# Performance work log

Hardware: AMD Instinct MI355X
Metric: run time of the kernel (lower is better)

Reference implementation:

```python
import jax, jax.numpy as jnp
import numpy as np

STRIDE = 4
HEADS = 8
KSIZE = 5
PAD_L = 4  # causal: kernel_size - 1


def _layernorm(x, g, b, eps=1e-5):
    mu = jnp.mean(x, axis=-1, keepdims=True)
    var = jnp.mean((x - mu) ** 2, axis=-1, keepdims=True)
    return (x - mu) * jax.lax.rsqrt(var + eps) * g + b


def setup_inputs() -> dict:
    key = jax.random.key(0)
    ks = jax.random.split(key, 6)
    B, T, C = 8, 2048, 1024
    D = 4096
    x = jax.random.normal(ks[0], (B, T, C), dtype=jnp.float32)
    W_proj = jax.random.normal(ks[1], (C * STRIDE, D), dtype=jnp.float32) * 0.02
    b_proj = jnp.zeros((D,), dtype=jnp.float32)
    ln_g = jnp.ones((D,), dtype=jnp.float32)
    ln_b = jnp.zeros((D,), dtype=jnp.float32)
    W_wgen = jax.random.normal(ks[2], (D, HEADS * KSIZE), dtype=jnp.float32) * 0.02
    b_wgen = jnp.zeros((HEADS * KSIZE,), dtype=jnp.float32)
    W_ff = jax.random.normal(ks[3], (D, D), dtype=jnp.float32) * 0.02
    b_ff = jnp.zeros((D,), dtype=jnp.float32)
    return {"x": x, "W_proj": W_proj, "b_proj": b_proj, "ln_g": ln_g, "ln_b": ln_b,
            "W_wgen": W_wgen, "b_wgen": b_wgen, "W_ff": W_ff, "b_ff": b_ff}


def reference(x, W_proj, b_proj, ln_g, ln_b, W_wgen, b_wgen, W_ff, b_ff):
    B, T, C = x.shape
    folded_T = T // STRIDE
    # fold time into channels, then dense projection to llm_dim
    xf = x[:, : folded_T * STRIDE].reshape(B, folded_T, C * STRIDE)
    h = xf @ W_proj + b_proj  # [B, Tf, D]
    D = h.shape[-1]
    R = D // HEADS
    # LConv1DBlock with norm_before + dynamic conv + (linear, relu, dropout p=0) + residual
    res = h
    y = _layernorm(h, ln_g, ln_b)
    # per-position dynamic weights, softmax over kernel taps
    w = (y @ W_wgen + b_wgen).reshape(B, folded_T, HEADS, KSIZE)
    w = jax.nn.softmax(w, axis=-1)  # [B, Tf, H, K]
    # causal depthwise conv: out[t] = sum_k w[t,k] * y[t - (K-1) + k]
    yp = jnp.pad(y, ((0, 0), (PAD_L, 0), (0, 0)))  # left pad time
    # stacked taps: [K, B, Tf, H, R]
    taps = jnp.stack([yp[:, k:k + folded_T] for k in range(KSIZE)], axis=0)
    taps = taps.reshape(KSIZE, B, folded_T, HEADS, R)
    conv = jnp.einsum('kbthr,bthk->bthr', taps, w).reshape(B, folded_T, D)
    # feed-forward ops: linear -> relu -> dropout(p=0)
    out = res + jax.nn.relu(conv @ W_ff + b_ff)
    return out
```

## Files before the change

### kernel.cpp

```cpp
#include <hip/hip_runtime.h>

typedef unsigned short u16;
typedef unsigned int u32;
typedef __attribute__((ext_vector_type(8))) short bf16x8;
typedef __attribute__((ext_vector_type(4))) float f32x4;

__device__ __forceinline__ float bf2f(u16 u) {
    union { u32 i; float f; } x; x.i = ((u32)u) << 16; return x.f;
}
__device__ __forceinline__ u16 f2bf(float f) {
    union { float f; u32 i; } x; x.f = f;
    u32 u = x.i;
    u += 0x7FFFu + ((u >> 16) & 1u);
    return (u16)(u >> 16);
}
__device__ __forceinline__ float wred(float v) {
    #pragma unroll
    for (int off = 32; off; off >>= 1) v += __shfl_down(v, off);
    return v;
}
__device__ __forceinline__ void gload_lds16(const void* g, void* l) {
    __builtin_amdgcn_global_load_lds(
        (const __attribute__((address_space(1))) u32*)g,
        (__attribute__((address_space(3))) u32*)l,
        16, 0, 0);
}

__global__ __launch_bounds__(256)
void prep(const float* __restrict__ x, u16* __restrict__ xb,
          const float* __restrict__ Wp, u16* __restrict__ WpT,
          const float* __restrict__ Wf, u16* __restrict__ WfT,
          const float* __restrict__ Wg, float* __restrict__ WgT) {
    __shared__ float tile[64][65];
    int b = blockIdx.x;
    int tid = threadIdx.x;
    if (b < 16384) {
        int i = (b * 256 + tid) * 4;
        float4 v = *(const float4*)(x + i);
        ushort4 p;
        p.x = f2bf(v.x); p.y = f2bf(v.y); p.z = f2bf(v.z); p.w = f2bf(v.w);
        *(ushort4*)(xb + i) = p;
    } else if (b < 24576) {
        const float* W = (b < 20480) ? Wp : Wf;
        u16* Wt = (b < 20480) ? WpT : WfT;
        int bid = (b < 20480) ? (b - 16384) : (b - 20480);
        int n0 = (bid & 63) * 64;
        int k0 = (bid >> 6) * 64;
        int tx = tid & 31, ty = tid >> 5;
        #pragma unroll
        for (int i = 0; i < 8; ++i) {
            int kk = ty + i * 8;
            const float* src = W + (size_t)(k0 + kk) * 4096 + n0;
            tile[kk][tx]      = src[tx];
            tile[kk][tx + 32] = src[tx + 32];
        }
        __syncthreads();
        #pragma unroll
        for (int i = 0; i < 8; ++i) {
            int nn = ty + i * 8;
            ushort2 p;
            p.x = f2bf(tile[tx * 2][nn]);
            p.y = f2bf(tile[tx * 2 + 1][nn]);
            *(ushort2*)(Wt + (size_t)(n0 + nn) * 4096 + k0 + tx * 2) = p;
        }
    } else {
        int idx = (b - 24576) * 256 + tid;
        int c = idx >> 12, e = idx & 4095;
        WgT[idx] = Wg[(size_t)e * 40 + c];
    }
}

template <int MODE>
__global__ __launch_bounds__(512, 2)
void gemm256(const u16* __restrict__ A, const u16* __restrict__ Bt,
             const float* __restrict__ bias, const void* __restrict__ res,
             void* __restrict__ outv) {
    const int K = 4096, N = 4096;
    __shared__ u16 smem[65536];

    const int tid = threadIdx.x;
    const int lane = tid & 63;
    const int w = tid >> 6;
    const int wr = w >> 2, wc = w & 3;
    const int fr = lane & 15;
    const int fk = (lane >> 4) * 8;
    const int cswz = (fr & 7) << 3;

    const int bid = blockIdx.x;
    const int swz = (bid & 7) * (gridDim.x >> 3) + (bid >> 3);
    const int tm = swz >> 4, tn = swz & 15;
    const size_t rowA0 = (size_t)tm * 256;
    const size_t rowB0 = (size_t)tn * 256;

    const int srl = lane >> 3;
    const int scl = ((lane & 7) ^ srl) << 3;

    f32x4 acc[8][4] = {};
    bf16x8 af[8];
    bf16x8 bh0[4];
    bf16x8 bh1[4];

    auto stA = [&](int b, int half, int kt) {
        #pragma unroll
        for (int i = 0; i < 2; ++i) {
            size_t grow = rowA0 + half * 128 + i * 64 + w * 8 + srl;
            gload_lds16(A + grow * K + kt * 64 + scl,
                        &smem[b * 32768 + half * 8192 + i * 4096 + w * 512 + lane * 8]);
        }
    };
    auto stB = [&](int b, int half, int kt) {
        #pragma unroll
        for (int i = 0; i < 2; ++i) {
            size_t grow = rowB0 + half * 128 + i * 64 + w * 8 + srl;
            gload_lds16(Bt + grow * K + kt * 64 + scl,
                        &smem[b * 32768 + 16384 + half * 8192 + i * 4096 + w * 512 + lane * 8]);
        }
    };
    auto ldA = [&](int b, int qm) {
        #pragma unroll
        for (int kk = 0; kk < 2; ++kk)
            #pragma unroll
            for (int m = 0; m < 4; ++m) {
                int base = b * 32768 + (wr * 128 + (qm * 4 + m) * 16 + fr) * 64;
                af[m * 2 + kk] = *(const bf16x8*)&smem[base + ((kk * 32 + fk) ^ cswz)];
            }
    };
    auto ldB = [&](int b, int qn, bf16x8 (&bh)[4]) {
        #pragma unroll
        for (int kk = 0; kk < 2; ++kk)
            #pragma unroll
            for (int n = 0; n < 2; ++n) {
                int base = b * 32768 + 16384 + (wc * 64 + qn * 32 + n * 16 + fr) * 64;
                bh[n * 2 + kk] = *(const bf16x8*)&smem[base + ((kk * 32 + fk) ^ cswz)];
            }
    };
    auto ldAB = [&](int b, int qm, int qn, bf16x8 (&bh)[4]) {
        #pragma unroll
        for (int kk = 0; kk < 2; ++kk) {
            #pragma unroll
            for (int m = 0; m < 4; ++m) {
                int base = b * 32768 + (wr * 128 + (qm * 4 + m) * 16 + fr) * 64;
                af[m * 2 + kk] = *(const bf16x8*)&smem[base + ((kk * 32 + fk) ^ cswz)];
            }
            #pragma unroll
            for (int n = 0; n < 2; ++n) {
                int base = b * 32768 + 16384 + (wc * 64 + qn * 32 + n * 16 + fr) * 64;
                bh[n * 2 + kk] = *(const bf16x8*)&smem[base + ((kk * 32 + fk) ^ cswz)];
            }
        }
    };
    auto mma = [&](int qm, int qn, bf16x8 (&bh)[4]) {
        __builtin_amdgcn_s_setprio(1);
        #pragma unroll
        for (int kk = 0; kk < 2; ++kk)
            #pragma unroll
            for (int m = 0; m < 4; ++m)
                #pragma unroll
                for (int n = 0; n < 2; ++n)
                    acc[qm*4+m][qn*2+n] = __builtin_amdgcn_mfma_f32_16x16x32_bf16(
                        af[m*2+kk], bh[n*2+kk], acc[qm*4+m][qn*2+n], 0, 0, 0);
        __builtin_amdgcn_s_setprio(0);
    };
    #define BAR() __builtin_amdgcn_s_barrier()
    #define VM4() asm volatile("s_waitcnt vmcnt(4)" ::: "memory")

    stB(0, 0, 0); stB(0, 1, 0); stA(0, 0, 0); stA(0, 1, 0);
    stB(1, 0, 1); stB(1, 1, 1);
    VM4();
    BAR();

    for (int i = 0; i < 32; ++i) {
        const int t = 2 * i;
        const int kt2 = (t + 2 < 64) ? t + 2 : 63;
        const int kt3 = (t + 3 < 64) ? t + 3 : 63;
        ldAB(0, 0, 0, bh0);
        stA(1, 0, t + 1);
        BAR(); mma(0, 0, bh0);
        ldB(0, 1, bh1);
        stA(1, 1, t + 1);
        BAR(); mma(0, 1, bh1);
        ldA(0, 1);
        stB(0, 0, kt2);
        BAR(); mma(1, 1, bh1);
        stB(0, 1, kt2);
        VM4();
        BAR(); mma(1, 0, bh0);
        ldAB(1, 0, 0, bh0);
        stA(0, 0, kt2);
        BAR(); mma(0, 0, bh0);
        ldB(1, 1, bh1);
        stA(0, 1, kt2);
        BAR(); mma(0, 1, bh1);
        ldA(1, 1);
        stB(1, 0, kt3);
        BAR(); mma(1, 1, bh1);
        stB(1, 1, kt3);
        VM4();
        BAR(); mma(1, 0, bh0);
    }
    #undef BAR
    #undef VM4

    const int cc = lane & 15;
    const int cr = (lane >> 4) * 4;
    if (MODE == 2) {
        __builtin_amdgcn_s_barrier();
        #pragma unroll
        for (int m = 0; m < 8; ++m) {
            #pragma unroll
            for (int n = 0; n < 4; ++n) {
                int lc = wc * 64 + n * 16 + cc;
                float bv = bias[rowB0 + lc];
                #pragma unroll
                for (int q = 0; q < 4; ++q) {
                    int lr = wr * 128 + m * 16 + cr + q;
                    int sc = (lc & 7) | (((lc >> 3) ^ (lr & 7)) << 3);
                    smem[lr * 256 + sc] = f2bf(acc[m][n][q] + bv);
                }
            }
        }
        __builtin_amdgcn_s_barrier();
        u16* ob = (u16*)outv;
        #pragma unroll
        for (int it = 0; it < 16; ++it) {
            int idx = it * 512 + tid;
            int lr = idx >> 5;
            int c16 = idx & 31;
            uint4 v = *(uint4*)&smem[lr * 256 + ((c16 ^ (lr & 7)) * 8)];
            *(uint4*)(ob + (rowA0 + lr) * (size_t)N + rowB0 + c16 * 8) = v;
        }
    } else {
        #pragma unroll
        for (int m = 0; m < 8; ++m) {
            #pragma unroll
            for (int n = 0; n < 4; ++n) {
                size_t row = rowA0 + wr * 128 + m * 16 + cr;
                size_t col = rowB0 + wc * 64 + n * 16 + cc;
                float bv = bias[col];
                #pragma unroll
                for (int q = 0; q < 4; ++q) {
                    size_t idx = (row + q) * (size_t)N + col;
                    float v = acc[m][n][q] + bv;
                    if (MODE == 1) v = ((const float*)res)[idx] + fmaxf(v, 0.0f);
                    if (MODE == 3) v = bf2f(((const u16*)res)[idx]) + fmaxf(v, 0.0f);
                    ((float*)outv)[idx] = v;
                }
            }
        }
    }
}

template <bool HB>
__global__ __launch_bounds__(256)
void ln_conv(const void* __restrict__ hv, const float* __restrict__ g,
             const float* __restrict__ beta, const float* __restrict__ WgT,
             const float* __restrict__ bg, u16* __restrict__ conv) {
    __shared__ u32 ylp[8][2048];
    __shared__ float red[8];
    __shared__ float wraw[8][40];
    __shared__ float wsm[8][40];
    __shared__ float pmv[4][2];

    int tid = threadIdx.x, lane = tid & 63, wv = tid >> 6;
    size_t row0 = (size_t)blockIdx.x * 8;
    int t0 = (int)(row0 & 511);

    for (int r = 0; r < 8; ++r) {
        float vals[16];
        float s = 0.f, ss = 0.f;
        if (HB) {
            const u16* hr = (const u16*)hv + (row0 + r) * 4096;
            #pragma unroll
            for (int i = 0; i < 2; ++i) {
                uint4 u = *(const uint4*)(hr + (size_t)(tid + i * 256) * 8);
                const u16* us = (const u16*)&u;
                #pragma unroll
                for (int j = 0; j < 8; ++j) {
                    float f = bf2f(us[j]);
                    vals[i * 8 + j] = f;
                    s += f; ss += f * f;
                }
            }
        } else {
            const float4* hr = (const float4*)((const float*)hv + (row0 + r) * 4096);
            #pragma unroll
            for (int i = 0; i < 4; ++i) {
                float4 v = hr[tid + i * 256];
                vals[i*4+0] = v.x; vals[i*4+1] = v.y; vals[i*4+2] = v.z; vals[i*4+3] = v.w;
                s  += v.x + v.y + v.z + v.w;
                ss += v.x*v.x + v.y*v.y + v.z*v.z + v.w*v.w;
            }
        }
        s = wred(s); ss = wred(ss);
        if (lane == 0) { red[wv] = s; red[4 + wv] = ss; }
        __syncthreads();
        float S = red[0] + red[1] + red[2] + red[3];
        float SS = red[4] + red[5] + red[6] + red[7];
        float mu = S * (1.0f / 4096.0f);
        float var = SS * (1.0f / 4096.0f) - mu * mu;
        float inv = rsqrtf(var + 1e-5f);
        if (HB) {
            #pragma unroll
            for (int i = 0; i < 2; ++i) {
                int e0 = i * 2048 + tid * 8;
                #pragma unroll
                for (int k = 0; k < 4; ++k) {
                    float2 gv = *(const float2*)(g + e0 + k * 2);
                    float2 bv = *(const float2*)(beta + e0 + k * 2);
                    float o0 = (vals[i*8 + k*2]     - mu) * inv * gv.x + bv.x;
                    float o1 = (vals[i*8 + k*2 + 1] - mu) * inv * gv.y + bv.y;
                    ylp[r][e0 / 2 + k] = (u32)f2bf(o0) | ((u32)f2bf(o1) << 16);
                }
            }
        } else {
            #pragma unroll
            for (int i = 0; i < 4; ++i) {
                int base = tid + i * 256;
                float4 gv = ((const float4*)g)[base];
                float4 bv = ((const float4*)beta)[base];
                float o0 = (vals[i*4+0] - mu) * inv * gv.x + bv.x;
                float o1 = (vals[i*4+1] - mu) * inv * gv.y + bv.y;
                float o2 = (vals[i*4+2] - mu) * inv * gv.z + bv.z;
                float o3 = (vals[i*4+3] - mu) * inv * gv.w + bv.w;
                ylp[r][base * 2]     = (u32)f2bf(o0) | ((u32)f2bf(o1) << 16);
                ylp[r][base * 2 + 1] = (u32)f2bf(o2) | ((u32)f2bf(o3) << 16);
            }
        }
        __syncthreads();
    }

    if (t0 > 0) {
        for (int r = 0; r < 4; ++r) {
            size_t row = row0 - 4 + r;
            float s = 0.f, ss = 0.f;
            if (HB) {
                const u16* hr = (const u16*)hv + row * 4096;
                #pragma unroll
                for (int i = 0; i < 2; ++i) {
                    uint4 u = *(const uint4*)(hr + (size_t)(tid + i * 256) * 8);
                    const u16* us = (const u16*)&u;
                    #pragma unroll
                    for (int j = 0; j < 8; ++j) { float f = bf2f(us[j]); s += f; ss += f * f; }
                }
            } else {
                const float4* hr = (const float4*)((const float*)hv + row * 4096);
                #pragma unroll
                for (int i = 0; i < 4; ++i) {
                    float4 v = hr[tid + i * 256];
                    s  += v.x + v.y + v.z + v.w;
                    ss += v.x*v.x + v.y*v.y + v.z*v.z + v.w*v.w;
                }
            }
            s = wred(s); ss = wred(ss);
            if (lane == 0) { red[wv] = s; red[4 + wv] = ss; }
            __syncthreads();
            if (tid == 0) {
                float S = red[0] + red[1] + red[2] + red[3];
                float SS = red[4] + red[5] + red[6] + red[7];
                float mu = S * (1.0f / 4096.0f);
                float var = SS * (1.0f / 4096.0f) - mu * mu;
                pmv[r][0] = mu;
                pmv[r][1] = rsqrtf(var + 1e-5f);
            }
            __syncthreads();
        }
    }

    float acc[8][10];
    #pragma unroll
    for (int r = 0; r < 8; ++r)
        #pragma unroll
        for (int c = 0; c < 10; ++c) acc[r][c] = 0.f;

    for (int eb = lane; eb < 2048; eb += 64) {
        float alo[8], ahi[8];
        #pragma unroll
        for (int r = 0; r < 8; ++r) {
            u32 a = ylp[r][eb];
            alo[r] = bf2f((u16)a);
            ahi[r] = bf2f((u16)(a >> 16));
        }
        #pragma unroll
        for (int c0 = 0; c0 < 10; ++c0) {
            int c = wv * 10 + c0;
            float2 wg = ((const float2*)(WgT + (size_t)c * 4096))[eb];
            #pragma unroll
            for (int r = 0; r < 8; ++r)
                acc[r][c0] += alo[r] * wg.x + ahi[r] * wg.y;
        }
    }
    #pragma unroll
    for (int r = 0; r < 8; ++r) {
        #pragma unroll
        for (int c0 = 0; c0 < 10; ++c0) {
            float p = wred(acc[r][c0]);
            if (lane == 0) wraw[r][wv * 10 + c0] = p + bg[wv * 10 + c0];
        }
    }
    __syncthreads();

    if (tid < 64) {
        int r = tid >> 3, hh = tid & 7;
        float e5[5];
        float mx = -1e30f;
        #pragma unroll
        for (int k = 0; k < 5; ++k) mx = fmaxf(mx, wraw[r][hh * 5 + k]);
        float sum = 0.f;
        #pragma unroll
        for (int k = 0; k < 5; ++k) { e5[k] = expf(wraw[r][hh * 5 + k] - mx); sum += e5[k]; }
        float isum = 1.0f / sum;
        #pragma unroll
        for (int k = 0; k < 5; ++k) wsm[r][hh * 5 + k] = e5[k] * isum;
    }
    __syncthreads();

    for (int half = 0; half < 2; ++half) {
        int d0 = half * 2048 + tid * 8;
        int head = d0 >> 9;
        float yp[4][8];
        #pragma unroll
        for (int r = 0; r < 4; ++r)
            #pragma unroll
            for (int e = 0; e < 8; ++e) yp[r][e] = 0.f;
        if (t0 > 0) {
            float gv[8], bv[8];
            #pragma unroll
            for (int k = 0; k < 2; ++k) {
                float4 gq = *(const float4*)(g + d0 + k * 4);
                float4 bq = *(const float4*)(beta + d0 + k * 4);
                gv[k*4+0]=gq.x; gv[k*4+1]=gq.y; gv[k*4+2]=gq.z; gv[k*4+3]=gq.w;
                bv[k*4+0]=bq.x; bv[k*4+1]=bq.y; bv[k*4+2]=bq.z; bv[k*4+3]=bq.w;
            }
            #pragma unroll
            for (int r = 0; r < 4; ++r) {
                float mu = pmv[r][0], inv = pmv[r][1];
                if (HB) {
                    uint4 u = *(const uint4*)((const u16*)hv + (row0 - 4 + r) * 4096 + d0);
                    const u16* us = (const u16*)&u;
                    #pragma unroll
                    for (int e = 0; e < 8; ++e)
                        yp[r][e] = bf2f(f2bf((bf2f(us[e]) - mu) * inv * gv[e] + bv[e]));
                } else {
                    const float* hr = (const float*)hv + (row0 - 4 + r) * 4096 + d0;
                    #pragma unroll
                    for (int e = 0; e < 8; ++e)
                        yp[r][e] = bf2f(f2bf((hr[e] - mu) * inv * gv[e] + bv[e]));
                }
            }
        }
        #pragma unroll
        for (int ri = 0; ri < 8; ++ri) {
            float a[8] = {0.f,0.f,0.f,0.f,0.f,0.f,0.f,0.f};
            #pragma unroll
            for (int k = 0; k < 5; ++k) {
                int src = ri - 4 + k;
                float w_ = wsm[ri][head * 5 + k];
                if (src >= 0) {
                    uint4 u = *(const uint4*)&ylp[src][d0 >> 1];
                    const u16* us = (const u16*)&u;
                    #pragma unroll
                    for (int e = 0; e < 8; ++e) a[e] += w_ * bf2f(us[e]);
                } else {
                    #pragma unroll
                    for (int e = 0; e < 8; ++e) a[e] += w_ * yp[src + 4][e];
                }
            }
            u16 o[8];
            #pragma unroll
            for (int e = 0; e < 8; ++e) o[e] = f2bf(a[e]);
            *(uint4*)(conv + (row0 + ri) * 4096 + d0) = *(uint4*)o;
        }
    }
}

extern "C" void kernel_launch(void* const* d_in, const int* in_sizes, int n_in,
                              void* d_out, int out_size, void* d_ws, size_t ws_size,
                              hipStream_t stream) {
    const float* x      = (const float*)d_in[0];
    const float* W_proj = (const float*)d_in[1];
    const float* b_proj = (const float*)d_in[2];
    const float* ln_g   = (const float*)d_in[3];
    const float* ln_b   = (const float*)d_in[4];
    const float* W_wgen = (const float*)d_in[5];
    const float* b_wgen = (const float*)d_in[6];
    const float* W_ff   = (const float*)d_in[7];
    const float* b_ff   = (const float*)d_in[8];
    float* out = (float*)d_out;

    char* ws = (char*)d_ws;
    u16* xb   = (u16*)(ws);
    u16* WpT  = (u16*)(ws + ((size_t)32 << 20));
    u16* WfT  = (u16*)(ws + ((size_t)64 << 20));
    float* WgT  = (float*)(ws + ((size_t)96 << 20));
    u16* hb   = (u16*)(ws + ((size_t)97 << 20));
    u16* conv = xb;

    prep<<<25216, 256, 0, stream>>>(x, xb, W_proj, WpT, W_ff, WfT, W_wgen, WgT);

    if (ws_size >= ((size_t)129 << 20)) {
        gemm256<2><<<256, 512, 0, stream>>>(xb, WpT, b_proj, nullptr, hb);
        ln_conv<true><<<512, 256, 0, stream>>>(hb, ln_g, ln_b, WgT, b_wgen, conv);
        gemm256<3><<<256, 512, 0, stream>>>(conv, WfT, b_ff, hb, out);
    } else {
        gemm256<0><<<256, 512, 0, stream>>>(xb, WpT, b_proj, nullptr, out);
        ln_conv<false><<<512, 256, 0, stream>>>(out, ln_g, ln_b, WgT, b_wgen, conv);
        gemm256<1><<<256, 512, 0, stream>>>(conv, WfT, b_ff, out, out);
    }
}
```

Before: 334.5 us.

## Compute dynamic conv weight projection with bf16 MFMA and swizzle LDS rows

```diff
diff --git a/kernel.cpp b/kernel.cpp
--- a/kernel.cpp
+++ b/kernel.cpp
@@ -30,7 +30,7 @@
 void prep(const float* __restrict__ x, u16* __restrict__ xb,
           const float* __restrict__ Wp, u16* __restrict__ WpT,
           const float* __restrict__ Wf, u16* __restrict__ WfT,
-          const float* __restrict__ Wg, float* __restrict__ WgT) {
+          const float* __restrict__ Wg, u16* __restrict__ WgTb) {
     __shared__ float tile[64][65];
     int b = blockIdx.x;
     int tid = threadIdx.x;
@@ -66,7 +66,7 @@
     } else {
         int idx = (b - 24576) * 256 + tid;
         int c = idx >> 12, e = idx & 4095;
-        WgT[idx] = Wg[(size_t)e * 40 + c];
+        WgTb[idx] = (c < 40) ? f2bf(Wg[(size_t)e * 40 + c]) : (u16)0;
     }
 }
 
@@ -253,13 +253,14 @@
 template <bool HB>
 __global__ __launch_bounds__(256)
 void ln_conv(const void* __restrict__ hv, const float* __restrict__ g,
-             const float* __restrict__ beta, const float* __restrict__ WgT,
+             const float* __restrict__ beta, const u16* __restrict__ WgTb,
              const float* __restrict__ bg, u16* __restrict__ conv) {
     __shared__ u32 ylp[8][2048];
     __shared__ float red[8];
     __shared__ float wraw[8][40];
     __shared__ float wsm[8][40];
     __shared__ float pmv[4][2];
+    __shared__ float pwg[4][3][8][16];
 
     int tid = threadIdx.x, lane = tid & 63, wv = tid >> 6;
     size_t row0 = (size_t)blockIdx.x * 8;
@@ -299,18 +300,23 @@
         float mu = S * (1.0f / 4096.0f);
         float var = SS * (1.0f / 4096.0f) - mu * mu;
         float inv = rsqrtf(var + 1e-5f);
+        const int rx = r << 2;
         if (HB) {
             #pragma unroll
             for (int i = 0; i < 2; ++i) {
-                int e0 = i * 2048 + tid * 8;
+                int w0 = (i * 1024 + tid * 4) ^ rx;
+                u32 words[4];
                 #pragma unroll
                 for (int k = 0; k < 4; ++k) {
-                    float2 gv = *(const float2*)(g + e0 + k * 2);
-                    float2 bv = *(const float2*)(beta + e0 + k * 2);
+                    int e0 = i * 2048 + tid * 8 + k * 2;
+                    float2 gv = *(const float2*)(g + e0);
+                    float2 bv = *(const float2*)(beta + e0);
                     float o0 = (vals[i*8 + k*2]     - mu) * inv * gv.x + bv.x;
                     float o1 = (vals[i*8 + k*2 + 1] - mu) * inv * gv.y + bv.y;
-                    ylp[r][e0 / 2 + k] = (u32)f2bf(o0) | ((u32)f2bf(o1) << 16);
-                }
+                    words[k] = (u32)f2bf(o0) | ((u32)f2bf(o1) << 16);
+                }
+                uint4 pk; pk.x = words[0]; pk.y = words[1]; pk.z = words[2]; pk.w = words[3];
+                *(uint4*)&ylp[r][w0] = pk;
             }
         } else {
             #pragma unroll
@@ -322,8 +328,9 @@
                 float o1 = (vals[i*4+1] - mu) * inv * gv.y + bv.y;
                 float o2 = (vals[i*4+2] - mu) * inv * gv.z + bv.z;
                 float o3 = (vals[i*4+3] - mu) * inv * gv.w + bv.w;
-                ylp[r][base * 2]     = (u32)f2bf(o0) | ((u32)f2bf(o1) << 16);
-                ylp[r][base * 2 + 1] = (u32)f2bf(o2) | ((u32)f2bf(o3) << 16);
+                int w0 = (base * 2) ^ rx;
+                ylp[r][w0]     = (u32)f2bf(o0) | ((u32)f2bf(o1) << 16);
+                ylp[r][w0 + 1] = (u32)f2bf(o2) | ((u32)f2bf(o3) << 16);
             }
         }
         __syncthreads();
@@ -366,36 +373,37 @@
         }
     }
 
-    float acc[8][10];
-    #pragma unroll
-    for (int r = 0; r < 8; ++r)
-        #pragma unroll
-        for (int c = 0; c < 10; ++c) acc[r][c] = 0.f;
-
-    for (int eb = lane; eb < 2048; eb += 64) {
-        float alo[8], ahi[8];
-        #pragma unroll
-        for (int r = 0; r < 8; ++r) {
-            u32 a = ylp[r][eb];
-            alo[r] = bf2f((u16)a);
-            ahi[r] = bf2f((u16)(a >> 16));
-        }
-        #pragma unroll
-        for (int c0 = 0; c0 < 10; ++c0) {
-            int c = wv * 10 + c0;
-            float2 wg = ((const float2*)(WgT + (size_t)c * 4096))[eb];
-            #pragma unroll
-            for (int r = 0; r < 8; ++r)
-                acc[r][c0] += alo[r] * wg.x + ahi[r] * wg.y;
-        }
-    }
-    #pragma unroll
-    for (int r = 0; r < 8; ++r) {
-        #pragma unroll
-        for (int c0 = 0; c0 < 10; ++c0) {
-            float p = wred(acc[r][c0]);
-            if (lane == 0) wraw[r][wv * 10 + c0] = p + bg[wv * 10 + c0];
-        }
+    {
+        f32x4 wacc[3] = {};
+        const int arow = lane & 7;
+        const int kofs = (lane >> 4) * 8;
+        const int ax = arow << 2;
+        #pragma unroll 4
+        for (int step = 0; step < 32; ++step) {
+            int kg = wv * 1024 + step * 32 + kofs;
+            bf16x8 ya = *(const bf16x8*)&ylp[arow][(kg >> 1) ^ ax];
+            #pragma unroll
+            for (int n = 0; n < 3; ++n) {
+                int col = n * 16 + (lane & 15);
+                bf16x8 wb = *(const bf16x8*)&WgTb[(size_t)col * 4096 + kg];
+                wacc[n] = __builtin_amdgcn_mfma_f32_16x16x32_bf16(ya, wb, wacc[n], 0, 0, 0);
+            }
+        }
+        if (lane < 32) {
+            int prow = (lane >> 4) * 4;
+            int pcol = lane & 15;
+            #pragma unroll
+            for (int n = 0; n < 3; ++n)
+                #pragma unroll
+                for (int q = 0; q < 4; ++q)
+                    pwg[wv][n][prow + q][pcol] = wacc[n][q];
+        }
+    }
+    __syncthreads();
+    for (int t = tid; t < 320; t += 256) {
+        int r = t / 40, c = t % 40;
+        wraw[r][c] = pwg[0][c >> 4][r][c & 15] + pwg[1][c >> 4][r][c & 15]
+                   + pwg[2][c >> 4][r][c & 15] + pwg[3][c >> 4][r][c & 15] + bg[c];
     }
     __syncthreads();
 
@@ -456,7 +464,7 @@
                 int src = ri - 4 + k;
                 float w_ = wsm[ri][head * 5 + k];
                 if (src >= 0) {
-                    uint4 u = *(const uint4*)&ylp[src][d0 >> 1];
+                    uint4 u = *(const uint4*)&ylp[src][(d0 >> 1) ^ (src << 2)];
                     const u16* us = (const u16*)&u;
                     #pragma unroll
                     for (int e = 0; e < 8; ++e) a[e] += w_ * bf2f(us[e]);
@@ -491,19 +499,19 @@
     u16* xb   = (u16*)(ws);
     u16* WpT  = (u16*)(ws + ((size_t)32 << 20));
     u16* WfT  = (u16*)(ws + ((size_t)64 << 20));
-    float* WgT  = (float*)(ws + ((size_t)96 << 20));
+    u16* WgTb = (u16*)(ws + ((size_t)96 << 20));
     u16* hb   = (u16*)(ws + ((size_t)97 << 20));
     u16* conv = xb;
 
-    prep<<<25216, 256, 0, stream>>>(x, xb, W_proj, WpT, W_ff, WfT, W_wgen, WgT);
+    prep<<<25344, 256, 0, stream>>>(x, xb, W_proj, WpT, W_ff, WfT, W_wgen, WgTb);
 
     if (ws_size >= ((size_t)129 << 20)) {
         gemm256<2><<<256, 512, 0, stream>>>(xb, WpT, b_proj, nullptr, hb);
-        ln_conv<true><<<512, 256, 0, stream>>>(hb, ln_g, ln_b, WgT, b_wgen, conv);
+        ln_conv<true><<<512, 256, 0, stream>>>(hb, ln_g, ln_b, WgTb, b_wgen, conv);
         gemm256<3><<<256, 512, 0, stream>>>(conv, WfT, b_ff, hb, out);
     } else {
         gemm256<0><<<256, 512, 0, stream>>>(xb, WpT, b_proj, nullptr, out);
-        ln_conv<false><<<512, 256, 0, stream>>>(out, ln_g, ln_b, WgT, b_wgen, conv);
+        ln_conv<false><<<512, 256, 0, stream>>>(out, ln_g, ln_b, WgTb, b_wgen, conv);
         gemm256<1><<<256, 512, 0, stream>>>(conv, WfT, b_ff, out, out);
     }
 }
```

Result: faster. 312.2 us, median of 2 (-6.7%).
